# Optimization experiments

Hardware: AMD Instinct MI355X
Metric: run time of the kernel (lower is better)

Reference implementation:

```python
import jax, jax.numpy as jnp
import numpy as np

NH, NKV, HD, PD = 16, 4, 128, 16  # heads, kv heads, head dim, rotary partial dim
BASE = 10000.0
QK_GAIN_INIT = 5.25


def _rms_norm(x):
    # F.rms_norm over last dim, eps = dtype eps (torch default when eps=None)
    return x * jax.lax.rsqrt(jnp.mean(x * x, axis=-1, keepdims=True) + jnp.finfo(x.dtype).eps)


def _rope_partial(x, cos, sin):
    # rotate first PD dims (two halves of PD//2), pass through the rest
    h = PD // 2
    x1, x2, xp = x[..., :h], x[..., h:PD], x[..., PD:]
    return jnp.concatenate([x1 * cos + x2 * sin, -x2 * cos + x1 * sin, xp], axis=-1)


def setup_inputs() -> dict:
    key = jax.random.key(0)
    ks = jax.random.split(key, 5)
    B, T, D = 2, 2048, 2048
    KD = NKV * HD
    s = 0.02
    return {
        "x": jax.random.normal(ks[0], (B, T, D), jnp.float32),
        "wq": jax.random.normal(ks[1], (D, D), jnp.float32) * s,
        "wk": jax.random.normal(ks[2], (KD, D), jnp.float32) * s,
        "wv": jax.random.normal(ks[3], (KD, D), jnp.float32) * s,
        "wp": jax.random.normal(ks[4], (D, D), jnp.float32) * s,
        "qg": jnp.full((NH,), QK_GAIN_INIT, jnp.float32),
    }


def reference(x, wq, wk, wv, wp, qg):
    B, T, D = x.shape
    q = (x @ wq.T).reshape(B, T, NH, HD)    # [B,T,NH,HD]
    k = (x @ wk.T).reshape(B, T, NKV, HD)   # [B,T,NKV,HD]
    v = (x @ wv.T).reshape(B, T, NKV, HD)
    q = _rms_norm(q)
    k = _rms_norm(k)
    # partial rotary tables: [T, PD//2] -> broadcast over head dim
    t = jnp.arange(T, dtype=jnp.float32)
    inv = 1.0 / (BASE ** (jnp.arange(0, PD, 2, dtype=jnp.float32) / PD))
    f = t[:, None] * inv[None, :]
    cos, sin = jnp.cos(f)[:, None, :], jnp.sin(f)[:, None, :]  # [T,1,PD//2]
    q = _rope_partial(q, cos, sin)
    k = _rope_partial(k, cos, sin)
    q = q * qg[None, None, :, None]         # learned per-head QK gain
    scale = 1.0 / jnp.sqrt(jnp.float32(HD))
    G = NH // NKV
    qh = q.reshape(B, T, NKV, G, HD)
    scores = jnp.einsum('bqkgd,bskd->bkgqs', qh, k) * scale  # [B,NKV,G,T,T]
    causal = jnp.arange(T)[:, None] >= jnp.arange(T)[None, :]
    scores = jnp.where(causal[None, None, None], scores, -jnp.inf)
    p = jax.nn.softmax(scores, axis=-1)
    y = jnp.einsum('bkgqs,bskd->bqkgd', p, v).reshape(B, T, D)
    return y @ wp.T
```

## Files before the change

### kernel.cpp

```cpp
#include <hip/hip_runtime.h>
#include <hip/hip_bf16.h>

#define B_   2
#define T_   2048
#define D_   2048
#define NH_  16
#define NKV_ 4
#define HD_  128
#define KD_  512
#define BT_  4096

typedef __bf16 bf16x8 __attribute__((ext_vector_type(8)));
typedef float  f32x4  __attribute__((ext_vector_type(4)));
typedef float  f32x16 __attribute__((ext_vector_type(16)));

__device__ __forceinline__ void gload_lds16(const __hip_bfloat16* g, __hip_bfloat16* l) {
    __builtin_amdgcn_global_load_lds(
        (__attribute__((address_space(1))) void*)(g),
        (__attribute__((address_space(3))) void*)(l),
        16, 0, 0);
}

__global__ void f2b_all(const float4* __restrict__ x,  const float4* __restrict__ wq,
                        const float4* __restrict__ wk, const float4* __restrict__ wv,
                        const float4* __restrict__ wp,
                        ushort4* __restrict__ xb,  ushort4* __restrict__ wqb,
                        ushort4* __restrict__ wkb, ushort4* __restrict__ wvb,
                        ushort4* __restrict__ wpb) {
    const int e0 = BT_ * D_ / 4;
    const int e1 = e0 + D_ * D_ / 4;
    const int e2 = e1 + KD_ * D_ / 4;
    const int e3 = e2 + KD_ * D_ / 4;
    const int e4 = e3 + D_ * D_ / 4;
    int idx = blockIdx.x * blockDim.x + threadIdx.x;
    int stride = gridDim.x * blockDim.x;
    for (int j = idx; j < e4; j += stride) {
        const float4* src; ushort4* dst; int off;
        if      (j < e0) { src = x;  dst = xb;  off = j; }
        else if (j < e1) { src = wq; dst = wqb; off = j - e0; }
        else if (j < e2) { src = wk; dst = wkb; off = j - e1; }
        else if (j < e3) { src = wv; dst = wvb; off = j - e2; }
        else             { src = wp; dst = wpb; off = j - e3; }
        float4 v = src[off];
        __hip_bfloat16 a = __float2bfloat16(v.x), b = __float2bfloat16(v.y),
                       c = __float2bfloat16(v.z), d = __float2bfloat16(v.w);
        ushort4 o;
        o.x = *(const unsigned short*)&a; o.y = *(const unsigned short*)&b;
        o.z = *(const unsigned short*)&c; o.w = *(const unsigned short*)&d;
        dst[off] = o;
    }
}

#define GEMM_PIPE(Aptr, Bptr, ROWB, colL, K)                                                  \
    const int tid = threadIdx.x, w = tid >> 6, lane = tid & 63;                               \
    const int lr = lane & 15, lk = lane >> 4;                                                 \
    const int wr = w >> 1, wc = w & 1;                                                        \
    const int lksw = lk ^ (lr & 3);                                                           \
    const size_t row0 = (size_t)(ROWB) * 128;                                                 \
    const int schunk = (tid % 4) ^ ((tid / 4) & 3);                                           \
    const __hip_bfloat16* ga = (Aptr) + (row0 + tid / 4) * (K) + schunk * 8;                  \
    const __hip_bfloat16* gb = (Bptr) + ((size_t)(colL) + tid / 4) * (K) + schunk * 8;        \
    const int KI = (K) >> 5;                                                                  \
    auto stage = [&](int u, int slot) {                                                       \
        int uu = u < KI ? u : KI - 1;                                                         \
        const int kk = uu * 32;                                                               \
        gload_lds16(ga + kk,                  &As[slot][w * 512]);                            \
        gload_lds16(ga + kk + (size_t)64*(K), &As[slot][2048 + w * 512]);                     \
        gload_lds16(gb + kk,                  &Bs[slot][w * 512]);                            \
        gload_lds16(gb + kk + (size_t)64*(K), &Bs[slot][2048 + w * 512]);                     \
    };                                                                                        \
    f32x4 acc[4][4] = {};                                                                     \
    stage(0, 0); stage(1, 1);                                                                 \
    int sstage = 2, scomp = 0;                                                                \
    for (int kt = 0; kt < KI; ++kt) {                                                         \
        stage(kt + 2, sstage);                                                                \
        asm volatile("s_waitcnt vmcnt(8)" ::: "memory");                                      \
        __builtin_amdgcn_s_barrier();                                                         \
        __builtin_amdgcn_sched_barrier(0);                                                    \
        bf16x8 af[4], bfr[4];                                                                 \
        _Pragma("unroll")                                                                     \
        for (int m = 0; m < 4; m++)                                                           \
            af[m] = *(const bf16x8*)&As[scomp][(wr * 64 + m * 16 + lr) * 32 + lksw * 8];      \
        _Pragma("unroll")                                                                     \
        for (int n = 0; n < 4; n++)                                                           \
            bfr[n] = *(const bf16x8*)&Bs[scomp][(wc * 64 + n * 16 + lr) * 32 + lksw * 8];     \
        _Pragma("unroll")                                                                     \
        for (int m = 0; m < 4; m++)                                                           \
            _Pragma("unroll")                                                                 \
            for (int n = 0; n < 4; n++)                                                       \
                acc[m][n] = __builtin_amdgcn_mfma_f32_16x16x32_bf16(af[m], bfr[n],            \
                                                                    acc[m][n], 0, 0, 0);      \
        asm volatile("s_waitcnt lgkmcnt(0)" ::: "memory");          \
        __builtin_amdgcn_sched_barrier(0);                                                    \
        __builtin_amdgcn_s_barrier();               \
        sstage = (sstage == 2) ? 0 : sstage + 1;                                              \
        scomp  = (scomp  == 2) ? 0 : scomp  + 1;                                              \
    }

__global__ __launch_bounds__(256, 3)
void gemm_qkv(const __hip_bfloat16* __restrict__ A,
              const __hip_bfloat16* __restrict__ Wq, const __hip_bfloat16* __restrict__ Wk,
              const __hip_bfloat16* __restrict__ Wv, const float* __restrict__ qg,
              __hip_bfloat16* __restrict__ qbb, __hip_bfloat16* __restrict__ kfb,
              __hip_bfloat16* __restrict__ vfb) {
    __shared__ __attribute__((aligned(16))) __hip_bfloat16 As[3][4096];
    __shared__ __attribute__((aligned(16))) __hip_bfloat16 Bs[3][4096];
    const int cb   = blockIdx.y;
    const int rowb = blockIdx.x;
    const __hip_bfloat16* Bw;
    if (cb < 16)      Bw = Wq + (size_t)cb * 128 * D_;
    else if (cb < 20) Bw = Wk + (size_t)(cb - 16) * 128 * D_;
    else              Bw = Wv + (size_t)(cb - 20) * 128 * D_;

    GEMM_PIPE(A, Bw, rowb, 0, D_)

    asm volatile("s_waitcnt vmcnt(0)" ::: "memory");
    __syncthreads();
    float* Red = (float*)&As[0][0];

    if (cb < 20) {
        float ssp[16];
        #pragma unroll
        for (int m = 0; m < 4; m++)
            #pragma unroll
            for (int r = 0; r < 4; r++) {
                float v = 0.f;
                #pragma unroll
                for (int n = 0; n < 4; n++) v += acc[m][n][r] * acc[m][n][r];
                #pragma unroll
                for (int off = 1; off < 16; off <<= 1) v += __shfl_xor(v, off);
                ssp[m * 4 + r] = v;
            }
        if (lr == 0) {
            #pragma unroll
            for (int m = 0; m < 4; m++)
                #pragma unroll
                for (int r = 0; r < 4; r++)
                    Red[wc * 128 + wr * 64 + m * 16 + lk * 4 + r] = ssp[m * 4 + r];
        }
        __syncthreads();
        #pragma unroll
        for (int m = 0; m < 4; m++)
            #pragma unroll
            for (int r = 0; r < 4; r++) {
                float tot = ssp[m * 4 + r] + Red[(wc ^ 1) * 128 + wr * 64 + m * 16 + lk * 4 + r];
                float rn = rsqrtf(tot * (1.0f / HD_) + 1.1920929e-7f);
                #pragma unroll
                for (int n = 0; n < 4; n++) acc[m][n][r] *= rn;
            }
        if (wc == 0) {
            float invf = exp2f(-(float)(lr & 7) * 1.66096404744368f);
            #pragma unroll
            for (int m = 0; m < 4; m++)
                #pragma unroll
                for (int r = 0; r < 4; r++) {
                    int t = (int)((row0 + wr * 64 + m * 16 + lk * 4 + r) & (T_ - 1));
                    float f = (float)t * invf;
                    float sn, cs;
                    sincosf(f, &sn, &cs);
                    float y  = acc[m][0][r];
                    float yp = __shfl_xor(y, 8);
                    acc[m][0][r] = (lr < 8) ? (y * cs + yp * sn) : (-y * cs + yp * sn);
                }
        }
    }

    if (cb < 16) {
        float g = qg[cb] * 0.1275174305f;
        #pragma unroll
        for (int m = 0; m < 4; m++)
            #pragma unroll
            for (int r = 0; r < 4; r++) {
                size_t bt = row0 + wr * 64 + m * 16 + lk * 4 + r;
                int b = (int)(bt >> 11), t = (int)(bt & (T_ - 1));
                __hip_bfloat16* dst = qbb + ((size_t)(b * NH_ + cb) * T_ + t) * HD_;
                #pragma unroll
                for (int n = 0; n < 4; n++) {
                    int d = wc * 64 + n * 16 + lr;
                    dst[d] = __float2bfloat16(acc[m][n][r] * g);
                }
            }
    } else if (cb < 20) {
        int kv = cb - 16;
        #pragma unroll
        for (int m = 0; m < 4; m++)
            #pragma unroll
            for (int r = 0; r < 4; r++) {
                size_t bt = row0 + wr * 64 + m * 16 + lk * 4 + r;
                int b = (int)(bt >> 11), t = (int)(bt & (T_ - 1));
                __hip_bfloat16* base = kfb + (size_t)(b * NKV_ + kv) * T_ * HD_;
                #pragma unroll
                for (int n = 0; n < 4; n++) {
                    int d = wc * 64 + n * 16 + lr;
                    size_t idx2 = (size_t)((((t >> 5) * 8 + (d >> 4)) * 2 + ((d >> 3) & 1))) * 256
                               + (t & 31) * 8 + (d & 7);
                    base[idx2] = __float2bfloat16(acc[m][n][r]);
                }
            }
    } else {
        int kv = cb - 20;
        #pragma unroll
        for (int m = 0; m < 4; m++)
            #pragma unroll
            for (int r = 0; r < 4; r++) {
                size_t bt = row0 + wr * 64 + m * 16 + lk * 4 + r;
                int b = (int)(bt >> 11), t = (int)(bt & (T_ - 1));
                __hip_bfloat16* base = vfb + (size_t)(b * NKV_ + kv) * T_ * HD_;
                #pragma unroll
                for (int n = 0; n < 4; n++) {
                    int d = wc * 64 + n * 16 + lr;
                    size_t idx2 = (size_t)(((((t >> 5) * 4 + (d >> 5)) * 4 + ((t >> 3) & 3)) * 32
                               + (d & 31))) * 8 + (t & 7);
                    base[idx2] = __float2bfloat16(acc[m][n][r]);
                }
            }
    }
}

__global__ __launch_bounds__(256, 3)
void gemm_p(const __hip_bfloat16* __restrict__ A, const __hip_bfloat16* __restrict__ B,
            float* __restrict__ C, int N, int K) {
    __shared__ __attribute__((aligned(16))) __hip_bfloat16 As[3][4096];
    __shared__ __attribute__((aligned(16))) __hip_bfloat16 Bs[3][4096];
    const int colL = blockIdx.y * 128;
    GEMM_PIPE(A, B, blockIdx.x, colL, K)
    #pragma unroll
    for (int m = 0; m < 4; m++)
        #pragma unroll
        for (int n = 0; n < 4; n++)
            #pragma unroll
            for (int r = 0; r < 4; r++)
                C[(row0 + wr * 64 + m * 16 + lk * 4 + r) * (size_t)N
                  + colL + wc * 64 + n * 16 + lr] = acc[m][n][r];
}

__device__ __forceinline__ unsigned pkbf(float a, float b) {
    __hip_bfloat16 x = __float2bfloat16(a), y = __float2bfloat16(b);
    unsigned short xu = *(const unsigned short*)&x, yu = *(const unsigned short*)&y;
    return (unsigned)xu | ((unsigned)yu << 16);
}

union U8u { unsigned u[4]; bf16x8 v; };

__global__ __launch_bounds__(512, 2)
void attn_fwd(const __hip_bfloat16* __restrict__ qb, const __hip_bfloat16* __restrict__ kfb,
              const __hip_bfloat16* __restrict__ vfb, __hip_bfloat16* __restrict__ yb) {
    __shared__ float Mrg[4][4224];
    const int tid  = threadIdx.x;
    const int w    = tid >> 6, lane = tid & 63;
    const int l31  = lane & 31, hi = lane >> 5;
    const int hd4  = w & 3;
    const int seg  = w >> 2;
    const int bid  = blockIdx.x;
    const int strm = bid & 7;
    const int b    = strm >> 2, kvh = strm & 3;
    const int i    = bid >> 3;
    const int h    = kvh * 4 + hd4;

    const __hip_bfloat16* kfp = kfb + (size_t)(b * NKV_ + kvh) * T_ * HD_ + lane * 8;
    const __hip_bfloat16* vfp = vfb + (size_t)(b * NKV_ + kvh) * T_ * HD_ + lane * 8;

    #pragma unroll
    for (int ph = 0; ph < 2; ++ph) {
        const int c  = (ph == 0) ? (63 - 2 * i) : (2 * i);
        const int ns = (c >> 1) + 1;
        const int qa = c * 32;

        const __hip_bfloat16* qp = qb + ((size_t)(b * NH_ + h) * T_ + qa) * HD_;
        bf16x8 qfr[8];
        #pragma unroll
        for (int hb = 0; hb < 8; ++hb)
            qfr[hb] = *(const bf16x8*)(qp + (size_t)l31 * HD_ + hb * 16 + hi * 8);

        f32x16 o0 = {}, o1 = {}, o2 = {}, o3 = {};
        float m = -1e30f, s = 0.f;

        bf16x8 kk[8], vv[8];
        {
            int kt0 = seg ? (ns <= c ? ns : c) : 0;
            #pragma unroll
            for (int hb = 0; hb < 8; ++hb)
                kk[hb] = *(const bf16x8*)(kfp + ((size_t)kt0 * 16 + hb * 2) * 256);
        }

        for (int t = 0; t < ns; ++t) {
            const int kt_raw = seg ? ns + t : t;
            const bool dead  = kt_raw > c;
            const int kt     = dead ? c : kt_raw;

            #pragma unroll
            for (int db = 0; db < 4; ++db) {
                vv[db * 2]     = *(const bf16x8*)(vfp + ((size_t)kt * 16 + db * 4) * 256);
                vv[db * 2 + 1] = *(const bf16x8*)(vfp + ((size_t)kt * 16 + db * 4) * 256 + 512);
            }

            f32x16 sa_a = {}, sa_b = {};
            __builtin_amdgcn_s_setprio(1);
            #pragma unroll
            for (int hb = 0; hb < 4; ++hb)
                sa_a = __builtin_amdgcn_mfma_f32_32x32x16_bf16(kk[hb], qfr[hb], sa_a, 0, 0, 0);
            #pragma unroll
            for (int hb = 4; hb < 8; ++hb)
                sa_b = __builtin_amdgcn_mfma_f32_32x32x16_bf16(kk[hb], qfr[hb], sa_b, 0, 0, 0);
            __builtin_amdgcn_s_setprio(0);
            f32x16 sa = sa_a + sa_b;

            {
                int ktn = seg * 0 + (seg ? ns : 0) + t + 1; if (ktn > c) ktn = c;
                #pragma unroll
                for (int hb = 0; hb < 8; ++hb)
                    kk[hb] = *(const bf16x8*)(kfp + ((size_t)ktn * 16 + hb * 2) * 256);
            }

            if (dead) {
                #pragma unroll
                for (int r = 0; r < 16; ++r) sa[r] = -1e30f;
            } else if (kt == c) {
                #pragma unroll
                for (int r = 0; r < 16; ++r) {
                    int kvrel = (r & 3) + 8 * (r >> 2) + 4 * hi;
                    if (kvrel > l31) sa[r] = -1e30f;
                }
            }
            float pm = sa[0];
            #pragma unroll
            for (int r = 1; r < 16; ++r) pm = fmaxf(pm, sa[r]);
            pm = fmaxf(pm, __shfl_xor(pm, 32));
            if (!__all(pm <= m + 8.f)) {
                float mn = fmaxf(m, pm);
                float corr = exp2f(m - mn);
                s *= corr;
                #pragma unroll
                for (int r = 0; r < 16; ++r) { o0[r] *= corr; o1[r] *= corr; o2[r] *= corr; o3[r] *= corr; }
                m = mn;
            }
            float p[16]; float rs = 0.f;
            #pragma unroll
            for (int r = 0; r < 16; ++r) { p[r] = exp2f(sa[r] - m); rs += p[r]; }
            rs += __shfl_xor(rs, 32);
            s += rs;
            unsigned pk[8];
            #pragma unroll
            for (int jj = 0; jj < 8; ++jj) pk[jj] = pkbf(p[2 * jj], p[2 * jj + 1]);
            unsigned pks[8];
            #pragma unroll
            for (int jj = 0; jj < 8; ++jj) pks[jj] = (unsigned)__shfl_xor((int)pk[jj], 32);
            U8u pa0, pa1;
            pa0.u[0] = hi ? pks[2] : pk[0];
            pa0.u[1] = hi ? pks[3] : pk[1];
            pa0.u[2] = hi ? pk[2]  : pks[0];
            pa0.u[3] = hi ? pk[3]  : pks[1];
            pa1.u[0] = hi ? pks[6] : pk[4];
            pa1.u[1] = hi ? pks[7] : pk[5];
            pa1.u[2] = hi ? pk[6]  : pks[4];
            pa1.u[3] = hi ? pk[7]  : pks[5];
            __builtin_amdgcn_s_setprio(1);
            o0 = __builtin_amdgcn_mfma_f32_32x32x16_bf16(vv[0], pa0.v, o0, 0, 0, 0);
            o0 = __builtin_amdgcn_mfma_f32_32x32x16_bf16(vv[1], pa1.v, o0, 0, 0, 0);
            o1 = __builtin_amdgcn_mfma_f32_32x32x16_bf16(vv[2], pa0.v, o1, 0, 0, 0);
            o1 = __builtin_amdgcn_mfma_f32_32x32x16_bf16(vv[3], pa1.v, o1, 0, 0, 0);
            o2 = __builtin_amdgcn_mfma_f32_32x32x16_bf16(vv[4], pa0.v, o2, 0, 0, 0);
            o2 = __builtin_amdgcn_mfma_f32_32x32x16_bf16(vv[5], pa1.v, o2, 0, 0, 0);
            o3 = __builtin_amdgcn_mfma_f32_32x32x16_bf16(vv[6], pa0.v, o3, 0, 0, 0);
            o3 = __builtin_amdgcn_mfma_f32_32x32x16_bf16(vv[7], pa1.v, o3, 0, 0, 0);
            __builtin_amdgcn_s_setprio(0);
        }

        __syncthreads();
        float* Mh = &Mrg[hd4][0];
        if (seg == 1) {
            #pragma unroll
            for (int r = 0; r < 16; ++r) {
                Mh[(0 * 16 + r) * 64 + lane] = o0[r];
                Mh[(1 * 16 + r) * 64 + lane] = o1[r];
                Mh[(2 * 16 + r) * 64 + lane] = o2[r];
                Mh[(3 * 16 + r) * 64 + lane] = o3[r];
            }
            Mh[4096 + lane] = m;
            Mh[4160 + lane] = s;
        }
        __syncthreads();
        if (seg == 0) {
            float m1 = Mh[4096 + lane], s1 = Mh[4160 + lane];
            float mn = fmaxf(m, m1);
            float ca = exp2f(m - mn), cb = exp2f(m1 - mn);
            s = s * ca + s1 * cb;
            #pragma unroll
            for (int r = 0; r < 16; ++r) {
                o0[r] = o0[r] * ca + Mh[(0 * 16 + r) * 64 + lane] * cb;
                o1[r] = o1[r] * ca + Mh[(1 * 16 + r) * 64 + lane] * cb;
                o2[r] = o2[r] * ca + Mh[(2 * 16 + r) * 64 + lane] * cb;
                o3[r] = o3[r] * ca + Mh[(3 * 16 + r) * 64 + lane] * cb;
            }
            float inv = 1.0f / s;
            __hip_bfloat16* yrow = yb + ((size_t)b * T_ + qa + l31) * D_ + h * HD_;
            #define WRITE_DB(ON, DB)                                                        \
                _Pragma("unroll")                                                           \
                for (int r4 = 0; r4 < 4; ++r4) {                                            \
                    ushort4 u;                                                              \
                    __hip_bfloat16 e0 = __float2bfloat16(ON[4*r4+0] * inv);                 \
                    __hip_bfloat16 e1 = __float2bfloat16(ON[4*r4+1] * inv);                 \
                    __hip_bfloat16 e2 = __float2bfloat16(ON[4*r4+2] * inv);                 \
                    __hip_bfloat16 e3 = __float2bfloat16(ON[4*r4+3] * inv);                 \
                    u.x = *(const unsigned short*)&e0; u.y = *(const unsigned short*)&e1;   \
                    u.z = *(const unsigned short*)&e2; u.w = *(const unsigned short*)&e3;   \
                    *(ushort4*)(yrow + (DB) * 32 + 8 * r4 + 4 * hi) = u;                    \
                }
            WRITE_DB(o0, 0) WRITE_DB(o1, 1) WRITE_DB(o2, 2) WRITE_DB(o3, 3)
            #undef WRITE_DB
        }
    }
}

extern "C" void kernel_launch(void* const* d_in, const int* in_sizes, int n_in,
                              void* d_out, int out_size, void* d_ws, size_t ws_size,
                              hipStream_t stream) {
    (void)in_sizes; (void)n_in; (void)out_size; (void)ws_size;
    const float* x  = (const float*)d_in[0];
    const float* wq = (const float*)d_in[1];
    const float* wk = (const float*)d_in[2];
    const float* wv = (const float*)d_in[3];
    const float* wp = (const float*)d_in[4];
    const float* qg = (const float*)d_in[5];
    float* out = (float*)d_out;

    char* ws = (char*)d_ws;
    size_t off = 0;
    auto alloc = [&](size_t bytes) { char* p = ws + off; off += (bytes + 255) & ~(size_t)255; return p; };

    __hip_bfloat16* xb  = (__hip_bfloat16*)alloc((size_t)BT_ * D_ * 2);
    __hip_bfloat16* wqb = (__hip_bfloat16*)alloc((size_t)D_ * D_ * 2);
    __hip_bfloat16* wkb = (__hip_bfloat16*)alloc((size_t)KD_ * D_ * 2);
    __hip_bfloat16* wvb = (__hip_bfloat16*)alloc((size_t)KD_ * D_ * 2);
    __hip_bfloat16* wpb = (__hip_bfloat16*)alloc((size_t)D_ * D_ * 2);
    __hip_bfloat16* qbb = (__hip_bfloat16*)alloc((size_t)BT_ * D_ * 2);
    __hip_bfloat16* kfb = (__hip_bfloat16*)alloc((size_t)BT_ * KD_ * 2);
    __hip_bfloat16* vfb = (__hip_bfloat16*)alloc((size_t)BT_ * KD_ * 2);
    __hip_bfloat16* ybb = xb;

    f2b_all<<<2048, 256, 0, stream>>>((const float4*)x, (const float4*)wq, (const float4*)wk,
                                      (const float4*)wv, (const float4*)wp,
                                      (ushort4*)xb, (ushort4*)wqb, (ushort4*)wkb,
                                      (ushort4*)wvb, (ushort4*)wpb);

    dim3 gqkv(BT_ / 128, 24);
    gemm_qkv<<<gqkv, 256, 0, stream>>>(xb, wqb, wkb, wvb, qg, qbb, kfb, vfb);

    attn_fwd<<<256, 512, 0, stream>>>(qbb, kfb, vfb, ybb);

    dim3 gp(BT_ / 128, D_ / 128);
    gemm_p<<<gp, 256, 0, stream>>>(ybb, wpb, out, D_, D_);
}
```

Baseline: 195.7 us.

## Split attention KV range across four segments and two heads per block

Each attention block now handles two query heads instead of four, with its eight waves split into four KV segments per head rather than two. The grid doubles to 512 blocks and launch bounds ask for four blocks per CU. The four partial softmax states are combined with a two-level tree merge through shared memory. The aim is more parallelism and shorter per-wave KV loops to better fill the GPU and balance causal work. The cost is extra merge passes and barriers, more K/V reloads because fewer heads share each block, and tighter register limits from the higher occupancy target.

After: 537.0 us. +174.4%, slower.

```diff
diff --git a/kernel.cpp b/kernel.cpp
--- a/kernel.cpp
+++ b/kernel.cpp
@@ -242,20 +242,21 @@
 
 union U8u { unsigned u[4]; bf16x8 v; };
 
-__global__ __launch_bounds__(512, 2)
+__global__ __launch_bounds__(512, 4)
 void attn_fwd(const __hip_bfloat16* __restrict__ qb, const __hip_bfloat16* __restrict__ kfb,
               const __hip_bfloat16* __restrict__ vfb, __hip_bfloat16* __restrict__ yb) {
-    __shared__ float Mrg[4][4224];
+    __shared__ float Mrg[2][2][4224];
     const int tid  = threadIdx.x;
     const int w    = tid >> 6, lane = tid & 63;
     const int l31  = lane & 31, hi = lane >> 5;
-    const int hd4  = w & 3;
-    const int seg  = w >> 2;
+    const int hd2  = w & 1;
+    const int seg  = w >> 1;
     const int bid  = blockIdx.x;
     const int strm = bid & 7;
     const int b    = strm >> 2, kvh = strm & 3;
-    const int i    = bid >> 3;
-    const int h    = kvh * 4 + hd4;
+    const int hp   = (bid >> 3) & 1;
+    const int i    = bid >> 4;
+    const int h    = kvh * 4 + hp * 2 + hd2;
 
     const __hip_bfloat16* kfp = kfb + (size_t)(b * NKV_ + kvh) * T_ * HD_ + lane * 8;
     const __hip_bfloat16* vfp = vfb + (size_t)(b * NKV_ + kvh) * T_ * HD_ + lane * 8;
@@ -263,7 +264,7 @@
     #pragma unroll
     for (int ph = 0; ph < 2; ++ph) {
         const int c  = (ph == 0) ? (63 - 2 * i) : (2 * i);
-        const int ns = (c >> 1) + 1;
+        const int ns = (c >> 2) + 1;
         const int qa = c * 32;
 
         const __hip_bfloat16* qp = qb + ((size_t)(b * NH_ + h) * T_ + qa) * HD_;
@@ -277,14 +278,14 @@
 
         bf16x8 kk[8], vv[8];
         {
-            int kt0 = seg ? (ns <= c ? ns : c) : 0;
+            int kt0 = seg * ns; if (kt0 > c) kt0 = c;
             #pragma unroll
             for (int hb = 0; hb < 8; ++hb)
                 kk[hb] = *(const bf16x8*)(kfp + ((size_t)kt0 * 16 + hb * 2) * 256);
         }
 
         for (int t = 0; t < ns; ++t) {
-            const int kt_raw = seg ? ns + t : t;
+            const int kt_raw = seg * ns + t;
             const bool dead  = kt_raw > c;
             const int kt     = dead ? c : kt_raw;
 
@@ -306,7 +307,7 @@
             f32x16 sa = sa_a + sa_b;
 
             {
-                int ktn = seg * 0 + (seg ? ns : 0) + t + 1; if (ktn > c) ktn = c;
+                int ktn = seg * ns + t + 1; if (ktn > c) ktn = c;
                 #pragma unroll
                 for (int hb = 0; hb < 8; ++hb)
                     kk[hb] = *(const bf16x8*)(kfp + ((size_t)ktn * 16 + hb * 2) * 256);
@@ -366,32 +367,45 @@
             __builtin_amdgcn_s_setprio(0);
         }
 
-        __syncthreads();
-        float* Mh = &Mrg[hd4][0];
-        if (seg == 1) {
+        auto writePart = [&](float* R) {
             #pragma unroll
             for (int r = 0; r < 16; ++r) {
-                Mh[(0 * 16 + r) * 64 + lane] = o0[r];
-                Mh[(1 * 16 + r) * 64 + lane] = o1[r];
-                Mh[(2 * 16 + r) * 64 + lane] = o2[r];
-                Mh[(3 * 16 + r) * 64 + lane] = o3[r];
-            }
-            Mh[4096 + lane] = m;
-            Mh[4160 + lane] = s;
-        }
-        __syncthreads();
-        if (seg == 0) {
-            float m1 = Mh[4096 + lane], s1 = Mh[4160 + lane];
+                R[(r)      * 64 + lane] = o0[r];
+                R[(16 + r) * 64 + lane] = o1[r];
+                R[(32 + r) * 64 + lane] = o2[r];
+                R[(48 + r) * 64 + lane] = o3[r];
+            }
+            R[4096 + lane] = m;
+            R[4160 + lane] = s;
+        };
+        auto mergePart = [&](const float* R) {
+            float m1 = R[4096 + lane], s1 = R[4160 + lane];
             float mn = fmaxf(m, m1);
             float ca = exp2f(m - mn), cb = exp2f(m1 - mn);
             s = s * ca + s1 * cb;
             #pragma unroll
             for (int r = 0; r < 16; ++r) {
-                o0[r] = o0[r] * ca + Mh[(0 * 16 + r) * 64 + lane] * cb;
-                o1[r] = o1[r] * ca + Mh[(1 * 16 + r) * 64 + lane] * cb;
-                o2[r] = o2[r] * ca + Mh[(2 * 16 + r) * 64 + lane] * cb;
-                o3[r] = o3[r] * ca + Mh[(3 * 16 + r) * 64 + lane] * cb;
-            }
+                o0[r] = o0[r] * ca + R[(r)      * 64 + lane] * cb;
+                o1[r] = o1[r] * ca + R[(16 + r) * 64 + lane] * cb;
+                o2[r] = o2[r] * ca + R[(32 + r) * 64 + lane] * cb;
+                o3[r] = o3[r] * ca + R[(48 + r) * 64 + lane] * cb;
+            }
+            m = mn;
+        };
+
+        float* R0 = &Mrg[hd2][0][0];
+        float* R1 = &Mrg[hd2][1][0];
+        __syncthreads();
+        if (seg == 1) writePart(R0);
+        if (seg == 3) writePart(R1);
+        __syncthreads();
+        if (seg == 0) mergePart(R0);
+        if (seg == 2) mergePart(R1);
+        __syncthreads();
+        if (seg == 2) writePart(R0);
+        __syncthreads();
+        if (seg == 0) {
+            mergePart(R0);
             float inv = 1.0f / s;
             __hip_bfloat16* yrow = yb + ((size_t)b * T_ + qa + l31) * D_ + h * HD_;
             #define WRITE_DB(ON, DB)                                                        \
@@ -446,7 +460,7 @@
     dim3 gqkv(BT_ / 128, 24);
     gemm_qkv<<<gqkv, 256, 0, stream>>>(xb, wqb, wkb, wvb, qg, qbb, kfb, vfb);
 
-    attn_fwd<<<256, 512, 0, stream>>>(qbb, kfb, vfb, ybb);
+    attn_fwd<<<512, 512, 0, stream>>>(qbb, kfb, vfb, ybb);
 
     dim3 gp(BT_ / 128, D_ / 128);
     gemm_p<<<gp, 256, 0, stream>>>(ybb, wpb, out, D_, D_);
```
